# Optimization experiments

Measured on AMD Instinct MI355X. Metric: run time of the kernel, lower is better.

## Reference

```python
import jax, jax.numpy as jnp
import numpy as np

N = 50000          # num nodes
E = 400000         # num edges
D_NODE = 128       # num_inputs_node
D_EDGE = 32        # num_inputs_edge
D_OUT = 128        # num_outputs
R = 16             # num_relations
B = 8              # num_bases


def setup_inputs() -> dict:
    key = jax.random.key(0)
    ks = jax.random.split(key, 12)
    s = 0.05  # small init scale (glorot-like)
    return {
        "vfts": jax.random.normal(ks[0], (N, D_NODE), dtype=jnp.float32),
        "adjs": jax.random.randint(ks[1], (2, E), 0, N, dtype=jnp.int32),
        "rels": jax.random.randint(ks[2], (E,), 0, R, dtype=jnp.int32),
        "embed_rels": jax.random.normal(ks[3], (E, D_EDGE), dtype=jnp.float32),
        "embed_rels_target": jax.random.normal(ks[4], (E, D_EDGE), dtype=jnp.float32),
        "weight": jax.random.normal(ks[5], (B, D_NODE, D_OUT), dtype=jnp.float32) * s,
        "comp": jax.random.normal(ks[6], (R, B), dtype=jnp.float32) * s,
        "attn_w1": jax.random.normal(ks[7], (2 * D_NODE + 2 * D_EDGE, D_OUT), dtype=jnp.float32) * s,
        "attn_b1": jnp.zeros((D_OUT,), dtype=jnp.float32),
        "attn_w2": jax.random.normal(ks[8], (D_OUT, 1), dtype=jnp.float32) * s,
        "attn_b2": jnp.zeros((1,), dtype=jnp.float32),
        "update": jax.random.normal(ks[9], (D_NODE, D_OUT), dtype=jnp.float32) * s,
    }


def reference(vfts, adjs, rels, embed_rels, embed_rels_target,
              weight, comp, attn_w1, attn_b1, attn_w2, attn_b2, update):
    src, dst = adjs[0], adjs[1]
    # per-edge attention: concat(src feat, dst feat, rel embed, rel-target embed) -> [E, 2*Dn+2*De]
    erps = jnp.concatenate((vfts[src], vfts[dst], embed_rels, embed_rels_target), axis=1)
    h = jax.nn.relu(erps @ attn_w1 + attn_b1)
    alphas = jax.nn.sigmoid(h @ attn_w2 + attn_b2)  # [E, 1]
    # basis-decomposed relation weights: [R, D_NODE, D_OUT]
    w_rel = (comp @ weight.reshape(B, D_NODE * D_OUT)).reshape(R, D_NODE, D_OUT)
    # dense broadcast matmul as in original: [R, N, D_OUT]
    srcs_dense = jnp.einsum('nd,rdo->rno', vfts, w_rel)
    # gather (rel, src) pairs, scale by alphas gathered BY RELATION INDEX (faithful to original alphas[rels])
    srcs = alphas[rels] * srcs_dense[rels, src]  # [E, D_OUT]
    vrps = jnp.zeros((vfts.shape[0], D_OUT), dtype=vfts.dtype)
    vrps = vrps.at[dst].add(srcs)
    dsts = vfts @ update  # [N, D_OUT]
    vrps = vrps.at[dst].add(dsts[dst])  # self-update added once per incoming edge
    return jax.nn.relu(vrps)
```

## Files before the change

### kernel.cpp

```cpp
#include <hip/hip_runtime.h>
#include <hip/hip_bf16.h>

#define D 128
#define DE 32
#define RNUM 16
#define BNUM 8
#define APAD 132
#define EPB 32
#define NBLK 256
#define PPART 32

typedef __attribute__((ext_vector_type(8))) short bfrag8;
typedef __attribute__((ext_vector_type(4))) float facc4;

__device__ inline unsigned short f2bf(float f) {
    union { float f; unsigned int u; } v; v.f = f;
    unsigned int u = v.u + 0x7FFFu + ((v.u >> 16) & 1u);
    return (unsigned short)(u >> 16);
}
__device__ inline float bf2f(unsigned short h) {
    union { unsigned int u; float f; } v; v.u = ((unsigned int)h) << 16; return v.f;
}

__global__ void k_wrel(const float* __restrict__ comp, const float* __restrict__ weight,
                       float* __restrict__ wrel) {
    int idx = blockIdx.x * blockDim.x + threadIdx.x;
    int total = RNUM * D * D;
    int stride = gridDim.x * blockDim.x;
    for (; idx < total; idx += stride) {
        int r = idx >> 14;
        int rest = idx & 16383;
        float s = 0.f;
#pragma unroll
        for (int b = 0; b < BNUM; ++b) s += comp[r * BNUM + b] * weight[b * 16384 + rest];
        wrel[idx] = s;
    }
}

__global__ void k_alphas(const float* __restrict__ vfts, const int* __restrict__ adjs,
                         const float* __restrict__ er, const float* __restrict__ ert,
                         const float* __restrict__ w1, const float* __restrict__ b1,
                         const float* __restrict__ w2, const float* __restrict__ b2,
                         float* __restrict__ alphas, int E) {
    __shared__ float erps[2 * D + 2 * DE];
    __shared__ float red[D];
    int e = blockIdx.x, t = threadIdx.x;
    int src = adjs[e], dst = adjs[E + e];
    erps[t] = vfts[src * D + t];
    erps[D + t] = vfts[dst * D + t];
    if (t < DE) {
        erps[2 * D + t] = er[e * DE + t];
        erps[2 * D + DE + t] = ert[e * DE + t];
    }
    __syncthreads();
    float h = b1[t];
    for (int k = 0; k < 2 * D + 2 * DE; ++k) h += erps[k] * w1[k * D + t];
    h = fmaxf(h, 0.f);
    red[t] = h * w2[t];
    __syncthreads();
    for (int s = 64; s > 0; s >>= 1) {
        if (t < s) red[t] += red[t + s];
        __syncthreads();
    }
    if (t == 0) alphas[e] = 1.f / (1.f + expf(-(red[0] + b2[0])));
}

__global__ void k_prep(const float* __restrict__ vfts, unsigned short* __restrict__ vb,
                       int total8) {
    int i = blockIdx.x * blockDim.x + threadIdx.x;
    int stride = gridDim.x * blockDim.x;
    for (; i < total8; i += stride) {
        float4 f0 = ((const float4*)vfts)[i * 2];
        float4 f1 = ((const float4*)vfts)[i * 2 + 1];
        bfrag8 v;
        v[0] = (short)f2bf(f0.x); v[1] = (short)f2bf(f0.y);
        v[2] = (short)f2bf(f0.z); v[3] = (short)f2bf(f0.w);
        v[4] = (short)f2bf(f1.x); v[5] = (short)f2bf(f1.y);
        v[6] = (short)f2bf(f1.z); v[7] = (short)f2bf(f1.w);
        ((bfrag8*)vb)[i] = v;
    }
}

__global__ void k_hist(const int* __restrict__ adjs, const int* __restrict__ rels, int E,
                       int* __restrict__ blockHist, int* __restrict__ indeg) {
    __shared__ int h[4][RNUM];
    int t = threadIdx.x;
    if (t < 4 * RNUM) ((int*)h)[t] = 0;
    __syncthreads();
    int w = t >> 6;
    int chunk = (E + NBLK - 1) / NBLK;
    int start = blockIdx.x * chunk;
    int end = min(start + chunk, E);
    for (int i = start + t; i < end; i += 256) {
        atomicAdd(&h[w][rels[i]], 1);
        atomicAdd(&indeg[adjs[E + i]], 1);
    }
    __syncthreads();
    if (t < RNUM)
        blockHist[blockIdx.x * RNUM + t] = h[0][t] + h[1][t] + h[2][t] + h[3][t];
}

__global__ void k_prefix2(const int* __restrict__ blockHist, int* __restrict__ basep,
                          int* __restrict__ blockBase) {
    __shared__ int hist[NBLK * RNUM];
    __shared__ int pre[NBLK * RNUM];
    __shared__ int bp[RNUM + 1];
    int t = threadIdx.x;
    for (int i = t; i < NBLK * RNUM; i += 256) hist[i] = blockHist[i];
    __syncthreads();
    if (t < RNUM) {
        int s = 0;
        for (int b = 0; b < NBLK; ++b) {
            pre[b * RNUM + t] = s;
            s += hist[b * RNUM + t];
        }
        bp[t] = s;
    }
    __syncthreads();
    if (t == 0) {
        int s = 0;
        for (int r = 0; r < RNUM; ++r) {
            int c = bp[r];
            bp[r] = s;
            basep[r] = s;
            s += c;
        }
        bp[RNUM] = s;
        basep[RNUM] = s;
    }
    __syncthreads();
    for (int i = t; i < NBLK * RNUM; i += 256)
        blockBase[i] = pre[i] + bp[i & (RNUM - 1)];
}

__global__ void k_scatter2(const int* __restrict__ rels, int E,
                           const int* __restrict__ blockBase, int* __restrict__ sorted) {
    __shared__ int pos[RNUM];
    int t = threadIdx.x;
    if (t < RNUM) pos[t] = blockBase[blockIdx.x * RNUM + t];
    __syncthreads();
    int chunk = (E + NBLK - 1) / NBLK;
    int start = blockIdx.x * chunk;
    int end = min(start + chunk, E);
    for (int i = start + t; i < end; i += 256) {
        int p = atomicAdd(&pos[rels[i]], 1);
        sorted[p] = i;
    }
}

__global__ void k_scanA(const int* __restrict__ indeg, int N, int* __restrict__ chunkSum) {
    __shared__ int sc[256];
    int t = threadIdx.x;
    int chunk = (N + NBLK - 1) / NBLK;
    int n0 = blockIdx.x * chunk;
    int v = (t < chunk && n0 + t < N) ? indeg[n0 + t] : 0;
    sc[t] = v;
    __syncthreads();
    for (int s = 128; s > 0; s >>= 1) {
        if (t < s) sc[t] += sc[t + s];
        __syncthreads();
    }
    if (t == 0) chunkSum[blockIdx.x] = sc[0];
}

__global__ void k_scanB(const int* __restrict__ chunkSum, int* __restrict__ chunkBase,
                        int* __restrict__ dstbase, int N) {
    if (threadIdx.x == 0) {
        int s = 0;
        for (int b = 0; b < NBLK; ++b) {
            chunkBase[b] = s;
            s += chunkSum[b];
        }
        dstbase[N] = s;
    }
}

__global__ void k_scanC(const int* __restrict__ indeg, int N,
                        const int* __restrict__ chunkBase, int* __restrict__ dstbase,
                        int* __restrict__ dpos) {
    __shared__ int sc[256];
    int t = threadIdx.x;
    int chunk = (N + NBLK - 1) / NBLK;
    int n0 = blockIdx.x * chunk;
    bool valid = (t < chunk) && (n0 + t < N);
    int v = valid ? indeg[n0 + t] : 0;
    sc[t] = v;
    __syncthreads();
    for (int ofs = 1; ofs < 256; ofs <<= 1) {
        int x = (t >= ofs) ? sc[t - ofs] : 0;
        __syncthreads();
        sc[t] += x;
        __syncthreads();
    }
    if (valid) {
        int excl = chunkBase[blockIdx.x] + sc[t] - v;
        dstbase[n0 + t] = excl;
        dpos[n0 + t] = excl;
    }
}

__global__ void k_dstpos(const int* __restrict__ adjs, const int* __restrict__ sorted, int E,
                         int* __restrict__ dpos, int* __restrict__ possorted) {
    int i = blockIdx.x * blockDim.x + threadIdx.x;
    int stride = gridDim.x * blockDim.x;
    for (; i < E; i += stride) {
        int eid = sorted[i];
        int dst = adjs[E + eid];
        possorted[i] = atomicAdd(&dpos[dst], 1);
    }
}

__global__ void __launch_bounds__(512)
k_edge(const unsigned short* __restrict__ vb, const int* __restrict__ adjs,
       const float* __restrict__ wrel, const float* __restrict__ alphas,
       const int* __restrict__ basep, const int* __restrict__ sorted,
       const int* __restrict__ possorted, unsigned short* __restrict__ srcs16, int E) {
    __shared__ unsigned short wt[D * D];
    __shared__ unsigned short at[EPB * D];
    __shared__ int esrc[EPB], epos[EPB];
    int t = threadIdx.x;
    int r = blockIdx.x / PPART;
    int bp = blockIdx.x % PPART;

    const float* wr = wrel + r * D * D;
    for (int i = t; i < D * D; i += 512) {
        int k = i >> 7, col = i & 127;
        int byte = (col << 8) + (k << 1);
        byte ^= (col & 7) << 4;
        *(unsigned short*)((char*)wt + byte) = f2bf(wr[i]);
    }
    float alpha = alphas[r];
    int s0 = basep[r], s1 = basep[r + 1];

    int lane = t & 63;
    int wave = t >> 6;
    int mtile = wave >> 2;
    int colbase = (wave & 3) << 5;
    int se = t >> 4;
    int skb = (t & 15) << 3;

    for (int off = s0 + bp * EPB; off < s1; off += PPART * EPB) {
        __syncthreads();
        if (t < EPB) {
            int idx = off + t;
            if (idx < s1) {
                int eid = sorted[idx];
                esrc[t] = adjs[eid];
                epos[t] = possorted[idx];
            } else {
                esrc[t] = 0;
                epos[t] = -1;
            }
        }
        __syncthreads();
        {
            bfrag8 v = *(const bfrag8*)(vb + (size_t)esrc[se] * D + skb);
            int byte = (se << 8) + (skb << 1);
            byte ^= (se & 7) << 4;
            *(bfrag8*)((char*)at + byte) = v;
        }
        __syncthreads();

        facc4 acc0 = {0.f, 0.f, 0.f, 0.f}, acc1 = {0.f, 0.f, 0.f, 0.f};
        int eb = (mtile << 4) + (lane & 15);
        int c0 = colbase + (lane & 15);
        int c1 = c0 + 16;
#pragma unroll
        for (int kk = 0; kk < 4; ++kk) {
            int kbase = (kk << 5) + ((lane >> 4) << 3);
            int ab = ((eb << 8) + (kbase << 1)) ^ ((eb & 7) << 4);
            bfrag8 a = *(const bfrag8*)((char*)at + ab);
            int b0 = ((c0 << 8) + (kbase << 1)) ^ ((c0 & 7) << 4);
            bfrag8 bv0 = *(const bfrag8*)((char*)wt + b0);
            int b1 = ((c1 << 8) + (kbase << 1)) ^ ((c1 & 7) << 4);
            bfrag8 bv1 = *(const bfrag8*)((char*)wt + b1);
            acc0 = __builtin_amdgcn_mfma_f32_16x16x32_bf16(a, bv0, acc0, 0, 0, 0);
            acc1 = __builtin_amdgcn_mfma_f32_16x16x32_bf16(a, bv1, acc1, 0, 0, 0);
        }
        int ebase = (mtile << 4) + ((lane >> 4) << 2);
#pragma unroll
        for (int j = 0; j < 4; ++j) {
            int p = epos[ebase + j];
            if (p >= 0) {
                unsigned short* q = srcs16 + (size_t)p * D + c0;
                q[0]  = f2bf(alpha * acc0[j]);
                q[16] = f2bf(alpha * acc1[j]);
            }
        }
    }
}

#define INIT_NODES 16
__global__ void __launch_bounds__(256)
k_final(const float* __restrict__ vfts, const float* __restrict__ update,
        const int* __restrict__ dstbase, const unsigned short* __restrict__ srcs16,
        float* __restrict__ out, int N) {
    __shared__ float upd[D * D];
    __shared__ float rows[INIT_NODES][APAD];
    int t = threadIdx.x;
    for (int idx = t; idx < D * D; idx += 256) upd[idx] = update[idx];
    int g = t >> 5;
    int cg = t & 31;
    for (int nb = blockIdx.x * INIT_NODES; nb < N; nb += gridDim.x * INIT_NODES) {
        __syncthreads();
        for (int idx = t; idx < INIT_NODES * D; idx += 256) {
            int nn = idx >> 7, k = idx & 127;
            int n = nb + nn;
            rows[nn][k] = (n < N) ? vfts[n * D + k] : 0.f;
        }
        __syncthreads();
        int n0 = g * 2, n1 = g * 2 + 1;
        float acc0[4] = {0, 0, 0, 0}, acc1[4] = {0, 0, 0, 0};
#pragma unroll 4
        for (int k = 0; k < D; ++k) {
            float4 w = *(const float4*)&upd[k * D + cg * 4];
            float a0 = rows[n0][k], a1 = rows[n1][k];
            acc0[0] += a0 * w.x; acc0[1] += a0 * w.y; acc0[2] += a0 * w.z; acc0[3] += a0 * w.w;
            acc1[0] += a1 * w.x; acc1[1] += a1 * w.y; acc1[2] += a1 * w.z; acc1[3] += a1 * w.w;
        }
        int na = nb + n0, nc = nb + n1;
        if (na < N) {
            int b0 = dstbase[na], b1 = dstbase[na + 1];
            float deg = (float)(b1 - b0);
            float r0 = deg * acc0[0], r1 = deg * acc0[1], r2 = deg * acc0[2], r3 = deg * acc0[3];
            for (int p = b0; p < b1; ++p) {
                ushort4 u = *(const ushort4*)(srcs16 + (size_t)p * D + cg * 4);
                r0 += bf2f(u.x); r1 += bf2f(u.y); r2 += bf2f(u.z); r3 += bf2f(u.w);
            }
            *(float4*)&out[(size_t)na * D + cg * 4] =
                make_float4(fmaxf(r0, 0.f), fmaxf(r1, 0.f), fmaxf(r2, 0.f), fmaxf(r3, 0.f));
        }
        if (nc < N) {
            int b0 = dstbase[nc], b1 = dstbase[nc + 1];
            float deg = (float)(b1 - b0);
            float r0 = deg * acc1[0], r1 = deg * acc1[1], r2 = deg * acc1[2], r3 = deg * acc1[3];
            for (int p = b0; p < b1; ++p) {
                ushort4 u = *(const ushort4*)(srcs16 + (size_t)p * D + cg * 4);
                r0 += bf2f(u.x); r1 += bf2f(u.y); r2 += bf2f(u.z); r3 += bf2f(u.w);
            }
            *(float4*)&out[(size_t)nc * D + cg * 4] =
                make_float4(fmaxf(r0, 0.f), fmaxf(r1, 0.f), fmaxf(r2, 0.f), fmaxf(r3, 0.f));
        }
    }
}

__global__ void k_init(const float* __restrict__ vfts, const float* __restrict__ update,
                       const int* __restrict__ indeg, float* __restrict__ out, int N) {
    __shared__ float upd[D * D];
    __shared__ float rows[INIT_NODES][APAD];
    int t = threadIdx.x;
    for (int idx = t; idx < D * D; idx += 256) upd[idx] = update[idx];
    int g = t >> 5;
    int cg = t & 31;
    for (int nb = blockIdx.x * INIT_NODES; nb < N; nb += gridDim.x * INIT_NODES) {
        __syncthreads();
        for (int idx = t; idx < INIT_NODES * D; idx += 256) {
            int nn = idx >> 7, k = idx & 127;
            int n = nb + nn;
            rows[nn][k] = (n < N) ? vfts[n * D + k] : 0.f;
        }
        __syncthreads();
        int n0 = g * 2, n1 = g * 2 + 1;
        float acc0[4] = {0, 0, 0, 0}, acc1[4] = {0, 0, 0, 0};
#pragma unroll 4
        for (int k = 0; k < D; ++k) {
            float4 w = *(const float4*)&upd[k * D + cg * 4];
            float a0 = rows[n0][k], a1 = rows[n1][k];
            acc0[0] += a0 * w.x; acc0[1] += a0 * w.y; acc0[2] += a0 * w.z; acc0[3] += a0 * w.w;
            acc1[0] += a1 * w.x; acc1[1] += a1 * w.y; acc1[2] += a1 * w.z; acc1[3] += a1 * w.w;
        }
        int na = nb + n0, nc = nb + n1;
        if (na < N) {
            float deg = (float)indeg[na];
            *(float4*)&out[na * D + cg * 4] =
                make_float4(deg * acc0[0], deg * acc0[1], deg * acc0[2], deg * acc0[3]);
        }
        if (nc < N) {
            float deg = (float)indeg[nc];
            *(float4*)&out[nc * D + cg * 4] =
                make_float4(deg * acc1[0], deg * acc1[1], deg * acc1[2], deg * acc1[3]);
        }
    }
}

__global__ void __launch_bounds__(512)
k_edge_at(const float* __restrict__ vfts, const int* __restrict__ adjs,
          const float* __restrict__ wrel, const float* __restrict__ alphas,
          const int* __restrict__ basep, const int* __restrict__ sorted,
          float* __restrict__ out, int E) {
    __shared__ unsigned short wt[D * D];
    __shared__ unsigned short at[EPB * D];
    __shared__ int esrc[EPB], edst[EPB];
    int t = threadIdx.x;
    int r = blockIdx.x / PPART;
    int bp = blockIdx.x % PPART;
    const float* wr = wrel + r * D * D;
    for (int i = t; i < D * D; i += 512) {
        int k = i >> 7, col = i & 127;
        int byte = (col << 8) + (k << 1);
        byte ^= (col & 7) << 4;
        *(unsigned short*)((char*)wt + byte) = f2bf(wr[i]);
    }
    float alpha = alphas[r];
    int s0 = basep[r], s1 = basep[r + 1];
    int lane = t & 63;
    int wave = t >> 6;
    int mtile = wave >> 2;
    int colbase = (wave & 3) << 5;
    int se = t >> 4;
    int skb = (t & 15) << 3;
    for (int off = s0 + bp * EPB; off < s1; off += PPART * EPB) {
        __syncthreads();
        if (t < EPB) {
            int idx = off + t;
            if (idx < s1) {
                int eid = sorted[idx];
                esrc[t] = adjs[eid];
                edst[t] = adjs[E + eid];
            } else {
                esrc[t] = 0;
                edst[t] = -1;
            }
        }
        __syncthreads();
        {
            const float* sp = vfts + (size_t)esrc[se] * D + skb;
            float4 f0 = *(const float4*)sp;
            float4 f1 = *(const float4*)(sp + 4);
            bfrag8 v;
            v[0] = (short)f2bf(f0.x); v[1] = (short)f2bf(f0.y);
            v[2] = (short)f2bf(f0.z); v[3] = (short)f2bf(f0.w);
            v[4] = (short)f2bf(f1.x); v[5] = (short)f2bf(f1.y);
            v[6] = (short)f2bf(f1.z); v[7] = (short)f2bf(f1.w);
            int byte = (se << 8) + (skb << 1);
            byte ^= (se & 7) << 4;
            *(bfrag8*)((char*)at + byte) = v;
        }
        __syncthreads();
        facc4 acc0 = {0.f, 0.f, 0.f, 0.f}, acc1 = {0.f, 0.f, 0.f, 0.f};
        int eb = (mtile << 4) + (lane & 15);
        int c0 = colbase + (lane & 15);
        int c1 = c0 + 16;
#pragma unroll
        for (int kk = 0; kk < 4; ++kk) {
            int kbase = (kk << 5) + ((lane >> 4) << 3);
            int ab = ((eb << 8) + (kbase << 1)) ^ ((eb & 7) << 4);
            bfrag8 a = *(const bfrag8*)((char*)at + ab);
            int b0 = ((c0 << 8) + (kbase << 1)) ^ ((c0 & 7) << 4);
            bfrag8 bv0 = *(const bfrag8*)((char*)wt + b0);
            int b1 = ((c1 << 8) + (kbase << 1)) ^ ((c1 & 7) << 4);
            bfrag8 bv1 = *(const bfrag8*)((char*)wt + b1);
            acc0 = __builtin_amdgcn_mfma_f32_16x16x32_bf16(a, bv0, acc0, 0, 0, 0);
            acc1 = __builtin_amdgcn_mfma_f32_16x16x32_bf16(a, bv1, acc1, 0, 0, 0);
        }
        int ebase = (mtile << 4) + ((lane >> 4) << 2);
#pragma unroll
        for (int j = 0; j < 4; ++j) {
            int d = edst[ebase + j];
            if (d >= 0) {
                float* p = out + (size_t)d * D + c0;
                atomicAdd(p, alpha * acc0[j]);
                atomicAdd(p + 16, alpha * acc1[j]);
            }
        }
    }
}

__global__ void k_relu(float* __restrict__ out, int total4) {
    int i = blockIdx.x * blockDim.x + threadIdx.x;
    int stride = gridDim.x * blockDim.x;
    for (; i < total4; i += stride) {
        float4 v = ((float4*)out)[i];
        v.x = fmaxf(v.x, 0.f);
        v.y = fmaxf(v.y, 0.f);
        v.z = fmaxf(v.z, 0.f);
        v.w = fmaxf(v.w, 0.f);
        ((float4*)out)[i] = v;
    }
}

extern "C" void kernel_launch(void* const* d_in, const int* in_sizes, int n_in,
                              void* d_out, int out_size, void* d_ws, size_t ws_size,
                              hipStream_t stream) {
    const float* vfts   = (const float*)d_in[0];
    const int*   adjs   = (const int*)d_in[1];
    const int*   rels   = (const int*)d_in[2];
    const float* er     = (const float*)d_in[3];
    const float* ert    = (const float*)d_in[4];
    const float* weight = (const float*)d_in[5];
    const float* comp   = (const float*)d_in[6];
    const float* w1     = (const float*)d_in[7];
    const float* b1     = (const float*)d_in[8];
    const float* w2     = (const float*)d_in[9];
    const float* b2     = (const float*)d_in[10];
    const float* update = (const float*)d_in[11];
    float* out = (float*)d_out;

    int N = in_sizes[0] / D;
    int E = in_sizes[2];
    int Nr = (N + 63) & ~63;

    char* ws = (char*)d_ws;
    size_t o = 0;
    float* wrel = (float*)(ws + o);            o += (size_t)RNUM * D * D * 4;
    float* alphas = (float*)(ws + o);          o += 256;
    unsigned short* vb = (unsigned short*)(ws + o);     o += (size_t)N * D * 2;
    o = (o + 255) & ~(size_t)255;
    unsigned short* srcs16 = (unsigned short*)(ws + o); o += (size_t)E * D * 2;
    o = (o + 255) & ~(size_t)255;
    int* basep     = (int*)(ws + o);           o += 128;
    int* indeg     = (int*)(ws + o);           o += (size_t)Nr * 4;
    int* blockHist = (int*)(ws + o);           o += (size_t)NBLK * RNUM * 4;
    int* blockBase = (int*)(ws + o);           o += (size_t)NBLK * RNUM * 4;
    int* sorted    = (int*)(ws + o);           o += (size_t)E * 4;
    int* chunkSum  = (int*)(ws + o);           o += NBLK * 4;
    int* chunkBase = (int*)(ws + o);           o += NBLK * 4;
    int* dstbase   = (int*)(ws + o);           o += (size_t)(Nr + 64) * 4;
    int* dpos      = (int*)(ws + o);           o += (size_t)Nr * 4;
    int* possorted = (int*)(ws + o);           o += (size_t)E * 4;
    bool big = (o <= ws_size);

    if (big) {
        hipMemsetAsync(indeg, 0, (size_t)Nr * 4, stream);
        k_wrel<<<256, 256, 0, stream>>>(comp, weight, wrel);
        k_alphas<<<RNUM, D, 0, stream>>>(vfts, adjs, er, ert, w1, b1, w2, b2, alphas, E);
        k_prep<<<1024, 256, 0, stream>>>(vfts, vb, N * D / 8);
        k_hist<<<NBLK, 256, 0, stream>>>(adjs, rels, E, blockHist, indeg);
        k_prefix2<<<1, 256, 0, stream>>>(blockHist, basep, blockBase);
        k_scatter2<<<NBLK, 256, 0, stream>>>(rels, E, blockBase, sorted);
        k_scanA<<<NBLK, 256, 0, stream>>>(indeg, N, chunkSum);
        k_scanB<<<1, 64, 0, stream>>>(chunkSum, chunkBase, dstbase, N);
        k_scanC<<<NBLK, 256, 0, stream>>>(indeg, N, chunkBase, dstbase, dpos);
        k_dstpos<<<256, 256, 0, stream>>>(adjs, sorted, E, dpos, possorted);
        k_edge<<<RNUM * PPART, 512, 0, stream>>>(vb, adjs, wrel, alphas, basep, sorted,
                                                 possorted, srcs16, E);
        k_final<<<512, 256, 0, stream>>>(vfts, update, dstbase, srcs16, out, N);
    } else {
        float* fwrel   = (float*)ws;
        float* falphas = (float*)(ws + (1 << 20));
        int* ib = (int*)(ws + (1 << 20) + 256);
        int* fbasep     = ib;
        int* findeg     = ib + 32;
        int* fblockHist = findeg + Nr;
        int* fblockBase = fblockHist + NBLK * RNUM;
        int* fsorted    = fblockBase + NBLK * RNUM;

        hipMemsetAsync(findeg, 0, (size_t)Nr * 4, stream);
        k_wrel<<<256, 256, 0, stream>>>(comp, weight, fwrel);
        k_alphas<<<RNUM, D, 0, stream>>>(vfts, adjs, er, ert, w1, b1, w2, b2, falphas, E);
        k_hist<<<NBLK, 256, 0, stream>>>(adjs, rels, E, fblockHist, findeg);
        k_prefix2<<<1, 256, 0, stream>>>(fblockHist, fbasep, fblockBase);
        k_scatter2<<<NBLK, 256, 0, stream>>>(rels, E, fblockBase, fsorted);
        k_init<<<512, 256, 0, stream>>>(vfts, update, findeg, out, N);
        k_edge_at<<<RNUM * PPART, 512, 0, stream>>>(vfts, adjs, fwrel, falphas, fbasep,
                                                    fsorted, out, E);
        k_relu<<<512, 256, 0, stream>>>(out, N * D / 4);
    }
}
```

Measured before the change: 379.7 us.

## Split final kernel into MFMA self-update GEMM and wave-per-node segment sum

The fused fp32 final kernel is replaced by two kernels. The first computes vfts@update with bf16 MFMA into the output buffer before the edge kernel runs. The second assigns one wave per destination node to sum its bf16 edge rows with coalesced 4-byte loads, adding degree times the stored self-update and applying ReLU. This moves the self-update off scalar fp32 FMAs and improves coalescing of the segment sum. In exchange it adds an extra write and read of the output, plus bf16 rounding of the self-update term.

Measured after the change: 321.4 us. 1.18x faster.

```diff
diff --git a/kernel.cpp b/kernel.cpp
--- a/kernel.cpp
+++ b/kernel.cpp
@@ -290,60 +290,93 @@
     }
 }
 
+__global__ void __launch_bounds__(512)
+k_dsts(const unsigned short* __restrict__ vb, const float* __restrict__ update,
+       float* __restrict__ out, int N) {
+    __shared__ unsigned short wt[D * D];
+    __shared__ unsigned short at[32 * D];
+    int t = threadIdx.x;
+    for (int i = t; i < D * D; i += 512) {
+        int k = i >> 7, col = i & 127;
+        int byte = (col << 8) + (k << 1);
+        byte ^= (col & 7) << 4;
+        *(unsigned short*)((char*)wt + byte) = f2bf(update[i]);
+    }
+    int lane = t & 63;
+    int wave = t >> 6;
+    int mtile = wave >> 2;
+    int colbase = (wave & 3) << 5;
+    int se = t >> 4;
+    int skb = (t & 15) << 3;
+    int nb = blockIdx.x * 32;
+    {
+        int n = nb + se;
+        if (n >= N) n = N - 1;
+        bfrag8 v = *(const bfrag8*)(vb + (size_t)n * D + skb);
+        int byte = ((se << 8) + (skb << 1)) ^ ((se & 7) << 4);
+        *(bfrag8*)((char*)at + byte) = v;
+    }
+    __syncthreads();
+    facc4 acc0 = {0.f, 0.f, 0.f, 0.f}, acc1 = {0.f, 0.f, 0.f, 0.f};
+    int eb = (mtile << 4) + (lane & 15);
+    int c0 = colbase + (lane & 15);
+    int c1 = c0 + 16;
+#pragma unroll
+    for (int kk = 0; kk < 4; ++kk) {
+        int kbase = (kk << 5) + ((lane >> 4) << 3);
+        int ab = ((eb << 8) + (kbase << 1)) ^ ((eb & 7) << 4);
+        bfrag8 a = *(const bfrag8*)((char*)at + ab);
+        int b0 = ((c0 << 8) + (kbase << 1)) ^ ((c0 & 7) << 4);
+        bfrag8 bv0 = *(const bfrag8*)((char*)wt + b0);
+        int b1 = ((c1 << 8) + (kbase << 1)) ^ ((c1 & 7) << 4);
+        bfrag8 bv1 = *(const bfrag8*)((char*)wt + b1);
+        acc0 = __builtin_amdgcn_mfma_f32_16x16x32_bf16(a, bv0, acc0, 0, 0, 0);
+        acc1 = __builtin_amdgcn_mfma_f32_16x16x32_bf16(a, bv1, acc1, 0, 0, 0);
+    }
+    int ebase = (mtile << 4) + ((lane >> 4) << 2);
+#pragma unroll
+    for (int j = 0; j < 4; ++j) {
+        int n = nb + ebase + j;
+        if (n < N) {
+            float* q = out + (size_t)n * D + c0;
+            q[0]  = acc0[j];
+            q[16] = acc1[j];
+        }
+    }
+}
+
+__global__ void __launch_bounds__(256)
+k_sum(const int* __restrict__ dstbase, const unsigned short* __restrict__ srcs16,
+      float* __restrict__ out, int N) {
+    int wid = (blockIdx.x * 256 + threadIdx.x) >> 6;
+    int lane = threadIdx.x & 63;
+    if (wid >= N) return;
+    int b0 = dstbase[wid], b1 = dstbase[wid + 1];
+    float deg = (float)(b1 - b0);
+    const unsigned int* base = (const unsigned int*)srcs16;
+    float a0 = 0.f, a1 = 0.f;
+    int p = b0;
+    for (; p + 4 <= b1; p += 4) {
+        unsigned int u0 = base[(size_t)(p + 0) * 64 + lane];
+        unsigned int u1 = base[(size_t)(p + 1) * 64 + lane];
+        unsigned int u2 = base[(size_t)(p + 2) * 64 + lane];
+        unsigned int u3 = base[(size_t)(p + 3) * 64 + lane];
+        a0 += bf2f((unsigned short)u0) + bf2f((unsigned short)u1) +
+              bf2f((unsigned short)u2) + bf2f((unsigned short)u3);
+        a1 += bf2f((unsigned short)(u0 >> 16)) + bf2f((unsigned short)(u1 >> 16)) +
+              bf2f((unsigned short)(u2 >> 16)) + bf2f((unsigned short)(u3 >> 16));
+    }
+    for (; p < b1; ++p) {
+        unsigned int u = base[(size_t)p * 64 + lane];
+        a0 += bf2f((unsigned short)u);
+        a1 += bf2f((unsigned short)(u >> 16));
+    }
+    float2* op = (float2*)out + (size_t)wid * 64 + lane;
+    float2 d = *op;
+    *op = make_float2(fmaxf(deg * d.x + a0, 0.f), fmaxf(deg * d.y + a1, 0.f));
+}
+
 #define INIT_NODES 16
-__global__ void __launch_bounds__(256)
-k_final(const float* __restrict__ vfts, const float* __restrict__ update,
-        const int* __restrict__ dstbase, const unsigned short* __restrict__ srcs16,
-        float* __restrict__ out, int N) {
-    __shared__ float upd[D * D];
-    __shared__ float rows[INIT_NODES][APAD];
-    int t = threadIdx.x;
-    for (int idx = t; idx < D * D; idx += 256) upd[idx] = update[idx];
-    int g = t >> 5;
-    int cg = t & 31;
-    for (int nb = blockIdx.x * INIT_NODES; nb < N; nb += gridDim.x * INIT_NODES) {
-        __syncthreads();
-        for (int idx = t; idx < INIT_NODES * D; idx += 256) {
-            int nn = idx >> 7, k = idx & 127;
-            int n = nb + nn;
-            rows[nn][k] = (n < N) ? vfts[n * D + k] : 0.f;
-        }
-        __syncthreads();
-        int n0 = g * 2, n1 = g * 2 + 1;
-        float acc0[4] = {0, 0, 0, 0}, acc1[4] = {0, 0, 0, 0};
-#pragma unroll 4
-        for (int k = 0; k < D; ++k) {
-            float4 w = *(const float4*)&upd[k * D + cg * 4];
-            float a0 = rows[n0][k], a1 = rows[n1][k];
-            acc0[0] += a0 * w.x; acc0[1] += a0 * w.y; acc0[2] += a0 * w.z; acc0[3] += a0 * w.w;
-            acc1[0] += a1 * w.x; acc1[1] += a1 * w.y; acc1[2] += a1 * w.z; acc1[3] += a1 * w.w;
-        }
-        int na = nb + n0, nc = nb + n1;
-        if (na < N) {
-            int b0 = dstbase[na], b1 = dstbase[na + 1];
-            float deg = (float)(b1 - b0);
-            float r0 = deg * acc0[0], r1 = deg * acc0[1], r2 = deg * acc0[2], r3 = deg * acc0[3];
-            for (int p = b0; p < b1; ++p) {
-                ushort4 u = *(const ushort4*)(srcs16 + (size_t)p * D + cg * 4);
-                r0 += bf2f(u.x); r1 += bf2f(u.y); r2 += bf2f(u.z); r3 += bf2f(u.w);
-            }
-            *(float4*)&out[(size_t)na * D + cg * 4] =
-                make_float4(fmaxf(r0, 0.f), fmaxf(r1, 0.f), fmaxf(r2, 0.f), fmaxf(r3, 0.f));
-        }
-        if (nc < N) {
-            int b0 = dstbase[nc], b1 = dstbase[nc + 1];
-            float deg = (float)(b1 - b0);
-            float r0 = deg * acc1[0], r1 = deg * acc1[1], r2 = deg * acc1[2], r3 = deg * acc1[3];
-            for (int p = b0; p < b1; ++p) {
-                ushort4 u = *(const ushort4*)(srcs16 + (size_t)p * D + cg * 4);
-                r0 += bf2f(u.x); r1 += bf2f(u.y); r2 += bf2f(u.z); r3 += bf2f(u.w);
-            }
-            *(float4*)&out[(size_t)nc * D + cg * 4] =
-                make_float4(fmaxf(r0, 0.f), fmaxf(r1, 0.f), fmaxf(r2, 0.f), fmaxf(r3, 0.f));
-        }
-    }
-}
-
 __global__ void k_init(const float* __restrict__ vfts, const float* __restrict__ update,
                        const int* __restrict__ indeg, float* __restrict__ out, int N) {
     __shared__ float upd[D * D];
@@ -532,9 +565,10 @@
         k_scanB<<<1, 64, 0, stream>>>(chunkSum, chunkBase, dstbase, N);
         k_scanC<<<NBLK, 256, 0, stream>>>(indeg, N, chunkBase, dstbase, dpos);
         k_dstpos<<<256, 256, 0, stream>>>(adjs, sorted, E, dpos, possorted);
+        k_dsts<<<(N + 31) / 32, 512, 0, stream>>>(vb, update, out, N);
         k_edge<<<RNUM * PPART, 512, 0, stream>>>(vb, adjs, wrel, alphas, basep, sorted,
                                                  possorted, srcs16, E);
-        k_final<<<512, 256, 0, stream>>>(vfts, update, dstbase, srcs16, out, N);
+        k_sum<<<(N + 3) / 4, 256, 0, stream>>>(dstbase, srcs16, out, N);
     } else {
         float* fwrel   = (float*)ws;
         float* falphas = (float*)(ws + (1 << 20));
```

## Aggregate basis-projected features per node then apply one concatenated basis GEMM

Applied to the files above, without the earlier changes.

Replaces the per-edge, per-relation matmul (sort by relation, compute E×128 projected rows, then sum per destination) with an algebraic reordering. Each destination node first sums its source features into 8 basis-coefficient-weighted accumulators, and one MFMA GEMM against the concatenated 8 basis weights plus the update matrix then produces the output. This removes the relation sort, the E×D bf16 intermediate buffer and the E-row matmul, cutting the matmul to N rows with K=9×128. The costs are a bf16 aggregation buffer of N×1024 and a rounding of the per-node sums to bf16 before the GEMM, which may change numerical accuracy.

Result: faster. 304.7 us (-19.8%).

```diff
diff --git a/kernel.cpp b/kernel.cpp
--- a/kernel.cpp
+++ b/kernel.cpp
@@ -20,21 +20,6 @@
 }
 __device__ inline float bf2f(unsigned short h) {
     union { unsigned int u; float f; } v; v.u = ((unsigned int)h) << 16; return v.f;
-}
-
-__global__ void k_wrel(const float* __restrict__ comp, const float* __restrict__ weight,
-                       float* __restrict__ wrel) {
-    int idx = blockIdx.x * blockDim.x + threadIdx.x;
-    int total = RNUM * D * D;
-    int stride = gridDim.x * blockDim.x;
-    for (; idx < total; idx += stride) {
-        int r = idx >> 14;
-        int rest = idx & 16383;
-        float s = 0.f;
-#pragma unroll
-        for (int b = 0; b < BNUM; ++b) s += comp[r * BNUM + b] * weight[b * 16384 + rest];
-        wrel[idx] = s;
-    }
 }
 
 __global__ void k_alphas(const float* __restrict__ vfts, const int* __restrict__ adjs,
@@ -65,6 +50,26 @@
     if (t == 0) alphas[e] = 1.f / (1.f + expf(-(red[0] + b2[0])));
 }
 
+__global__ void k_coef(const float* __restrict__ alphas, const float* __restrict__ comp,
+                       float* __restrict__ coef) {
+    int t = threadIdx.x;
+    if (t < RNUM * BNUM) coef[t] = alphas[t >> 3] * comp[t];
+}
+
+__global__ void k_wcat(const float* __restrict__ weight, const float* __restrict__ update,
+                       unsigned short* __restrict__ wcatT) {
+    int idx = blockIdx.x * blockDim.x + threadIdx.x;
+    int total = 9 * D * D;
+    int stride = gridDim.x * blockDim.x;
+    for (; idx < total; idx += stride) {
+        int s = idx >> 14;
+        int rest = idx & 16383;
+        int col = rest >> 7, k = rest & 127;
+        float v = (s < 8) ? weight[s * 16384 + k * D + col] : update[k * D + col];
+        wcatT[idx] = f2bf(v);
+    }
+}
+
 __global__ void k_prep(const float* __restrict__ vfts, unsigned short* __restrict__ vb,
                        int total8) {
     int i = blockIdx.x * blockDim.x + threadIdx.x;
@@ -81,6 +86,221 @@
     }
 }
 
+__global__ void k_indeg(const int* __restrict__ adjs, int E, int* __restrict__ indeg) {
+    int i = blockIdx.x * blockDim.x + threadIdx.x;
+    int stride = gridDim.x * blockDim.x;
+    for (; i < E; i += stride) atomicAdd(&indeg[adjs[E + i]], 1);
+}
+
+__global__ void k_scanA(const int* __restrict__ indeg, int N, int* __restrict__ chunkSum) {
+    __shared__ int sc[256];
+    int t = threadIdx.x;
+    int chunk = (N + NBLK - 1) / NBLK;
+    int n0 = blockIdx.x * chunk;
+    int v = (t < chunk && n0 + t < N) ? indeg[n0 + t] : 0;
+    sc[t] = v;
+    __syncthreads();
+    for (int s = 128; s > 0; s >>= 1) {
+        if (t < s) sc[t] += sc[t + s];
+        __syncthreads();
+    }
+    if (t == 0) chunkSum[blockIdx.x] = sc[0];
+}
+
+__global__ void k_scanB(const int* __restrict__ chunkSum, int* __restrict__ chunkBase,
+                        int* __restrict__ dstbase, int N) {
+    if (threadIdx.x == 0) {
+        int s = 0;
+        for (int b = 0; b < NBLK; ++b) {
+            chunkBase[b] = s;
+            s += chunkSum[b];
+        }
+        dstbase[N] = s;
+    }
+}
+
+__global__ void k_scanC(const int* __restrict__ indeg, int N,
+                        const int* __restrict__ chunkBase, int* __restrict__ dstbase,
+                        int* __restrict__ dpos) {
+    __shared__ int sc[256];
+    int t = threadIdx.x;
+    int chunk = (N + NBLK - 1) / NBLK;
+    int n0 = blockIdx.x * chunk;
+    bool valid = (t < chunk) && (n0 + t < N);
+    int v = valid ? indeg[n0 + t] : 0;
+    sc[t] = v;
+    __syncthreads();
+    for (int ofs = 1; ofs < 256; ofs <<= 1) {
+        int x = (t >= ofs) ? sc[t - ofs] : 0;
+        __syncthreads();
+        sc[t] += x;
+        __syncthreads();
+    }
+    if (valid) {
+        int excl = chunkBase[blockIdx.x] + sc[t] - v;
+        dstbase[n0 + t] = excl;
+        dpos[n0 + t] = excl;
+    }
+}
+
+__global__ void k_dstscatter(const int* __restrict__ adjs, const int* __restrict__ rels, int E,
+                             int* __restrict__ dpos, int2* __restrict__ srcrel) {
+    int i = blockIdx.x * blockDim.x + threadIdx.x;
+    int stride = gridDim.x * blockDim.x;
+    for (; i < E; i += stride) {
+        int dst = adjs[E + i];
+        int p = atomicAdd(&dpos[dst], 1);
+        srcrel[p] = make_int2(adjs[i], rels[i]);
+    }
+}
+
+__global__ void __launch_bounds__(256)
+k_agg(const unsigned short* __restrict__ vb, const int2* __restrict__ srcrel,
+      const int* __restrict__ dstbase, const float* __restrict__ coef,
+      unsigned short* __restrict__ aggc, int N) {
+    __shared__ float cs[RNUM * BNUM];
+    int t = threadIdx.x;
+    if (t < RNUM * BNUM) cs[t] = coef[t];
+    __syncthreads();
+    int wid = (blockIdx.x * 256 + t) >> 6;
+    int lane = t & 63;
+    if (wid >= N) return;
+    int b0 = dstbase[wid], b1 = dstbase[wid + 1];
+    const unsigned int* vbd = (const unsigned int*)vb;
+    float a0_0 = 0, a0_1 = 0, a1_0 = 0, a1_1 = 0, a2_0 = 0, a2_1 = 0, a3_0 = 0, a3_1 = 0;
+    float a4_0 = 0, a4_1 = 0, a5_0 = 0, a5_1 = 0, a6_0 = 0, a6_1 = 0, a7_0 = 0, a7_1 = 0;
+    int p = b0;
+    for (; p + 2 <= b1; p += 2) {
+        int2 sr0 = srcrel[p];
+        int2 sr1 = srcrel[p + 1];
+        unsigned int u0 = vbd[(size_t)sr0.x * 64 + lane];
+        unsigned int u1 = vbd[(size_t)sr1.x * 64 + lane];
+        float4 cA0 = *(const float4*)&cs[sr0.y * 8];
+        float4 cB0 = *(const float4*)&cs[sr0.y * 8 + 4];
+        float4 cA1 = *(const float4*)&cs[sr1.y * 8];
+        float4 cB1 = *(const float4*)&cs[sr1.y * 8 + 4];
+        float v0 = bf2f((unsigned short)u0), v1 = bf2f((unsigned short)(u0 >> 16));
+        float w0 = bf2f((unsigned short)u1), w1 = bf2f((unsigned short)(u1 >> 16));
+        a0_0 += cA0.x * v0 + cA1.x * w0; a0_1 += cA0.x * v1 + cA1.x * w1;
+        a1_0 += cA0.y * v0 + cA1.y * w0; a1_1 += cA0.y * v1 + cA1.y * w1;
+        a2_0 += cA0.z * v0 + cA1.z * w0; a2_1 += cA0.z * v1 + cA1.z * w1;
+        a3_0 += cA0.w * v0 + cA1.w * w0; a3_1 += cA0.w * v1 + cA1.w * w1;
+        a4_0 += cB0.x * v0 + cB1.x * w0; a4_1 += cB0.x * v1 + cB1.x * w1;
+        a5_0 += cB0.y * v0 + cB1.y * w0; a5_1 += cB0.y * v1 + cB1.y * w1;
+        a6_0 += cB0.z * v0 + cB1.z * w0; a6_1 += cB0.z * v1 + cB1.z * w1;
+        a7_0 += cB0.w * v0 + cB1.w * w0; a7_1 += cB0.w * v1 + cB1.w * w1;
+    }
+    if (p < b1) {
+        int2 sr0 = srcrel[p];
+        unsigned int u0 = vbd[(size_t)sr0.x * 64 + lane];
+        float4 cA0 = *(const float4*)&cs[sr0.y * 8];
+        float4 cB0 = *(const float4*)&cs[sr0.y * 8 + 4];
+        float v0 = bf2f((unsigned short)u0), v1 = bf2f((unsigned short)(u0 >> 16));
+        a0_0 += cA0.x * v0; a0_1 += cA0.x * v1;
+        a1_0 += cA0.y * v0; a1_1 += cA0.y * v1;
+        a2_0 += cA0.z * v0; a2_1 += cA0.z * v1;
+        a3_0 += cA0.w * v0; a3_1 += cA0.w * v1;
+        a4_0 += cB0.x * v0; a4_1 += cB0.x * v1;
+        a5_0 += cB0.y * v0; a5_1 += cB0.y * v1;
+        a6_0 += cB0.z * v0; a6_1 += cB0.z * v1;
+        a7_0 += cB0.w * v0; a7_1 += cB0.w * v1;
+    }
+    unsigned int* ob = (unsigned int*)(aggc + (size_t)wid * 1024);
+#define PACK(x, y) ((unsigned int)f2bf(x) | ((unsigned int)f2bf(y) << 16))
+    ob[0 * 64 + lane] = PACK(a0_0, a0_1);
+    ob[1 * 64 + lane] = PACK(a1_0, a1_1);
+    ob[2 * 64 + lane] = PACK(a2_0, a2_1);
+    ob[3 * 64 + lane] = PACK(a3_0, a3_1);
+    ob[4 * 64 + lane] = PACK(a4_0, a4_1);
+    ob[5 * 64 + lane] = PACK(a5_0, a5_1);
+    ob[6 * 64 + lane] = PACK(a6_0, a6_1);
+    ob[7 * 64 + lane] = PACK(a7_0, a7_1);
+#undef PACK
+}
+
+__global__ void __launch_bounds__(512)
+k_gemm(const unsigned short* __restrict__ aggc, const unsigned short* __restrict__ vb,
+       const unsigned short* __restrict__ wcatT, const int* __restrict__ dstbase,
+       float* __restrict__ out, int N) {
+    __shared__ unsigned short wt[D * D];
+    __shared__ unsigned short at[32 * D];
+    int t = threadIdx.x;
+    int lane = t & 63;
+    int wave = t >> 6;
+    int mtile = wave >> 2;
+    int colbase = (wave & 3) << 5;
+    int se = t >> 4;
+    int skb = (t & 15) << 3;
+    int nb = blockIdx.x * 32;
+    int nclamp = min(nb + se, N - 1);
+    facc4 accA0 = {0, 0, 0, 0}, accA1 = {0, 0, 0, 0};
+    facc4 accB0 = {0, 0, 0, 0}, accB1 = {0, 0, 0, 0};
+    int eb = (mtile << 4) + (lane & 15);
+    int c0 = colbase + (lane & 15);
+    int c1 = c0 + 16;
+    int wcol = t >> 4;
+    int wkb = (t & 15) << 3;
+    for (int s = 0; s < 9; ++s) {
+        __syncthreads();
+#pragma unroll
+        for (int q = 0; q < 4; ++q) {
+            int col = wcol + (q << 5);
+            bfrag8 v = *(const bfrag8*)(wcatT + (size_t)s * 16384 + col * D + wkb);
+            int byte = ((col << 8) + (wkb << 1)) ^ ((col & 7) << 4);
+            *(bfrag8*)((char*)wt + byte) = v;
+        }
+        {
+            const unsigned short* src = (s < 8)
+                ? aggc + (size_t)nclamp * 1024 + s * D + skb
+                : vb + (size_t)nclamp * D + skb;
+            bfrag8 v = *(const bfrag8*)src;
+            int byte = ((se << 8) + (skb << 1)) ^ ((se & 7) << 4);
+            *(bfrag8*)((char*)at + byte) = v;
+        }
+        __syncthreads();
+#pragma unroll
+        for (int kk = 0; kk < 4; ++kk) {
+            int kbase = (kk << 5) + ((lane >> 4) << 3);
+            bfrag8 a = *(const bfrag8*)((char*)at + (((eb << 8) + (kbase << 1)) ^ ((eb & 7) << 4)));
+            bfrag8 bv0 = *(const bfrag8*)((char*)wt + (((c0 << 8) + (kbase << 1)) ^ ((c0 & 7) << 4)));
+            bfrag8 bv1 = *(const bfrag8*)((char*)wt + (((c1 << 8) + (kbase << 1)) ^ ((c1 & 7) << 4)));
+            if (s < 8) {
+                accA0 = __builtin_amdgcn_mfma_f32_16x16x32_bf16(a, bv0, accA0, 0, 0, 0);
+                accA1 = __builtin_amdgcn_mfma_f32_16x16x32_bf16(a, bv1, accA1, 0, 0, 0);
+            } else {
+                accB0 = __builtin_amdgcn_mfma_f32_16x16x32_bf16(a, bv0, accB0, 0, 0, 0);
+                accB1 = __builtin_amdgcn_mfma_f32_16x16x32_bf16(a, bv1, accB1, 0, 0, 0);
+            }
+        }
+    }
+    int ebase = (mtile << 4) + ((lane >> 4) << 2);
+#pragma unroll
+    for (int j = 0; j < 4; ++j) {
+        int n = nb + ebase + j;
+        if (n < N) {
+            float deg = (float)(dstbase[n + 1] - dstbase[n]);
+            float* q = out + (size_t)n * D + c0;
+            q[0]  = fmaxf(accA0[j] + deg * accB0[j], 0.f);
+            q[16] = fmaxf(accA1[j] + deg * accB1[j], 0.f);
+        }
+    }
+}
+
+__global__ void k_wrel(const float* __restrict__ comp, const float* __restrict__ weight,
+                       float* __restrict__ wrel) {
+    int idx = blockIdx.x * blockDim.x + threadIdx.x;
+    int total = RNUM * D * D;
+    int stride = gridDim.x * blockDim.x;
+    for (; idx < total; idx += stride) {
+        int r = idx >> 14;
+        int rest = idx & 16383;
+        float s = 0.f;
+#pragma unroll
+        for (int b = 0; b < BNUM; ++b) s += comp[r * BNUM + b] * weight[b * 16384 + rest];
+        wrel[idx] = s;
+    }
+}
+
 __global__ void k_hist(const int* __restrict__ adjs, const int* __restrict__ rels, int E,
                        int* __restrict__ blockHist, int* __restrict__ indeg) {
     __shared__ int h[4][RNUM];
@@ -148,202 +368,7 @@
     }
 }
 
-__global__ void k_scanA(const int* __restrict__ indeg, int N, int* __restrict__ chunkSum) {
-    __shared__ int sc[256];
-    int t = threadIdx.x;
-    int chunk = (N + NBLK - 1) / NBLK;
-    int n0 = blockIdx.x * chunk;
-    int v = (t < chunk && n0 + t < N) ? indeg[n0 + t] : 0;
-    sc[t] = v;
-    __syncthreads();
-    for (int s = 128; s > 0; s >>= 1) {
-        if (t < s) sc[t] += sc[t + s];
-        __syncthreads();
-    }
-    if (t == 0) chunkSum[blockIdx.x] = sc[0];
-}
-
-__global__ void k_scanB(const int* __restrict__ chunkSum, int* __restrict__ chunkBase,
-                        int* __restrict__ dstbase, int N) {
-    if (threadIdx.x == 0) {
-        int s = 0;
-        for (int b = 0; b < NBLK; ++b) {
-            chunkBase[b] = s;
-            s += chunkSum[b];
-        }
-        dstbase[N] = s;
-    }
-}
-
-__global__ void k_scanC(const int* __restrict__ indeg, int N,
-                        const int* __restrict__ chunkBase, int* __restrict__ dstbase,
-                        int* __restrict__ dpos) {
-    __shared__ int sc[256];
-    int t = threadIdx.x;
-    int chunk = (N + NBLK - 1) / NBLK;
-    int n0 = blockIdx.x * chunk;
-    bool valid = (t < chunk) && (n0 + t < N);
-    int v = valid ? indeg[n0 + t] : 0;
-    sc[t] = v;
-    __syncthreads();
-    for (int ofs = 1; ofs < 256; ofs <<= 1) {
-        int x = (t >= ofs) ? sc[t - ofs] : 0;
-        __syncthreads();
-        sc[t] += x;
-        __syncthreads();
-    }
-    if (valid) {
-        int excl = chunkBase[blockIdx.x] + sc[t] - v;
-        dstbase[n0 + t] = excl;
-        dpos[n0 + t] = excl;
-    }
-}
-
-__global__ void k_dstpos(const int* __restrict__ adjs, const int* __restrict__ sorted, int E,
-                         int* __restrict__ dpos, int* __restrict__ possorted) {
-    int i = blockIdx.x * blockDim.x + threadIdx.x;
-    int stride = gridDim.x * blockDim.x;
-    for (; i < E; i += stride) {
-        int eid = sorted[i];
-        int dst = adjs[E + eid];
-        possorted[i] = atomicAdd(&dpos[dst], 1);
-    }
-}
-
-__global__ void __launch_bounds__(512)
-k_edge(const unsigned short* __restrict__ vb, const int* __restrict__ adjs,
-       const float* __restrict__ wrel, const float* __restrict__ alphas,
-       const int* __restrict__ basep, const int* __restrict__ sorted,
-       const int* __restrict__ possorted, unsigned short* __restrict__ srcs16, int E) {
-    __shared__ unsigned short wt[D * D];
-    __shared__ unsigned short at[EPB * D];
-    __shared__ int esrc[EPB], epos[EPB];
-    int t = threadIdx.x;
-    int r = blockIdx.x / PPART;
-    int bp = blockIdx.x % PPART;
-
-    const float* wr = wrel + r * D * D;
-    for (int i = t; i < D * D; i += 512) {
-        int k = i >> 7, col = i & 127;
-        int byte = (col << 8) + (k << 1);
-        byte ^= (col & 7) << 4;
-        *(unsigned short*)((char*)wt + byte) = f2bf(wr[i]);
-    }
-    float alpha = alphas[r];
-    int s0 = basep[r], s1 = basep[r + 1];
-
-    int lane = t & 63;
-    int wave = t >> 6;
-    int mtile = wave >> 2;
-    int colbase = (wave & 3) << 5;
-    int se = t >> 4;
-    int skb = (t & 15) << 3;
-
-    for (int off = s0 + bp * EPB; off < s1; off += PPART * EPB) {
-        __syncthreads();
-        if (t < EPB) {
-            int idx = off + t;
-            if (idx < s1) {
-                int eid = sorted[idx];
-                esrc[t] = adjs[eid];
-                epos[t] = possorted[idx];
-            } else {
-                esrc[t] = 0;
-                epos[t] = -1;
-            }
-        }
-        __syncthreads();
-        {
-            bfrag8 v = *(const bfrag8*)(vb + (size_t)esrc[se] * D + skb);
-            int byte = (se << 8) + (skb << 1);
-            byte ^= (se & 7) << 4;
-            *(bfrag8*)((char*)at + byte) = v;
-        }
-        __syncthreads();
-
-        facc4 acc0 = {0.f, 0.f, 0.f, 0.f}, acc1 = {0.f, 0.f, 0.f, 0.f};
-        int eb = (mtile << 4) + (lane & 15);
-        int c0 = colbase + (lane & 15);
-        int c1 = c0 + 16;
-#pragma unroll
-        for (int kk = 0; kk < 4; ++kk) {
-            int kbase = (kk << 5) + ((lane >> 4) << 3);
-            int ab = ((eb << 8) + (kbase << 1)) ^ ((eb & 7) << 4);
-            bfrag8 a = *(const bfrag8*)((char*)at + ab);
-            int b0 = ((c0 << 8) + (kbase << 1)) ^ ((c0 & 7) << 4);
-            bfrag8 bv0 = *(const bfrag8*)((char*)wt + b0);
-            int b1 = ((c1 << 8) + (kbase << 1)) ^ ((c1 & 7) << 4);
-            bfrag8 bv1 = *(const bfrag8*)((char*)wt + b1);
-            acc0 = __builtin_amdgcn_mfma_f32_16x16x32_bf16(a, bv0, acc0, 0, 0, 0);
-            acc1 = __builtin_amdgcn_mfma_f32_16x16x32_bf16(a, bv1, acc1, 0, 0, 0);
-        }
-        int ebase = (mtile << 4) + ((lane >> 4) << 2);
-#pragma unroll
-        for (int j = 0; j < 4; ++j) {
-            int p = epos[ebase + j];
-            if (p >= 0) {
-                unsigned short* q = srcs16 + (size_t)p * D + c0;
-                q[0]  = f2bf(alpha * acc0[j]);
-                q[16] = f2bf(alpha * acc1[j]);
-            }
-        }
-    }
-}
-
 #define INIT_NODES 16
-__global__ void __launch_bounds__(256)
-k_final(const float* __restrict__ vfts, const float* __restrict__ update,
-        const int* __restrict__ dstbase, const unsigned short* __restrict__ srcs16,
-        float* __restrict__ out, int N) {
-    __shared__ float upd[D * D];
-    __shared__ float rows[INIT_NODES][APAD];
-    int t = threadIdx.x;
-    for (int idx = t; idx < D * D; idx += 256) upd[idx] = update[idx];
-    int g = t >> 5;
-    int cg = t & 31;
-    for (int nb = blockIdx.x * INIT_NODES; nb < N; nb += gridDim.x * INIT_NODES) {
-        __syncthreads();
-        for (int idx = t; idx < INIT_NODES * D; idx += 256) {
-            int nn = idx >> 7, k = idx & 127;
-            int n = nb + nn;
-            rows[nn][k] = (n < N) ? vfts[n * D + k] : 0.f;
-        }
-        __syncthreads();
-        int n0 = g * 2, n1 = g * 2 + 1;
-        float acc0[4] = {0, 0, 0, 0}, acc1[4] = {0, 0, 0, 0};
-#pragma unroll 4
-        for (int k = 0; k < D; ++k) {
-            float4 w = *(const float4*)&upd[k * D + cg * 4];
-            float a0 = rows[n0][k], a1 = rows[n1][k];
-            acc0[0] += a0 * w.x; acc0[1] += a0 * w.y; acc0[2] += a0 * w.z; acc0[3] += a0 * w.w;
-            acc1[0] += a1 * w.x; acc1[1] += a1 * w.y; acc1[2] += a1 * w.z; acc1[3] += a1 * w.w;
-        }
-        int na = nb + n0, nc = nb + n1;
-        if (na < N) {
-            int b0 = dstbase[na], b1 = dstbase[na + 1];
-            float deg = (float)(b1 - b0);
-            float r0 = deg * acc0[0], r1 = deg * acc0[1], r2 = deg * acc0[2], r3 = deg * acc0[3];
-            for (int p = b0; p < b1; ++p) {
-                ushort4 u = *(const ushort4*)(srcs16 + (size_t)p * D + cg * 4);
-                r0 += bf2f(u.x); r1 += bf2f(u.y); r2 += bf2f(u.z); r3 += bf2f(u.w);
-            }
-            *(float4*)&out[(size_t)na * D + cg * 4] =
-                make_float4(fmaxf(r0, 0.f), fmaxf(r1, 0.f), fmaxf(r2, 0.f), fmaxf(r3, 0.f));
-        }
-        if (nc < N) {
-            int b0 = dstbase[nc], b1 = dstbase[nc + 1];
-            float deg = (float)(b1 - b0);
-            float r0 = deg * acc1[0], r1 = deg * acc1[1], r2 = deg * acc1[2], r3 = deg * acc1[3];
-            for (int p = b0; p < b1; ++p) {
-                ushort4 u = *(const ushort4*)(srcs16 + (size_t)p * D + cg * 4);
-                r0 += bf2f(u.x); r1 += bf2f(u.y); r2 += bf2f(u.z); r3 += bf2f(u.w);
-            }
-            *(float4*)&out[(size_t)nc * D + cg * 4] =
-                make_float4(fmaxf(r0, 0.f), fmaxf(r1, 0.f), fmaxf(r2, 0.f), fmaxf(r3, 0.f));
-        }
-    }
-}
-
 __global__ void k_init(const float* __restrict__ vfts, const float* __restrict__ update,
                        const int* __restrict__ indeg, float* __restrict__ out, int N) {
     __shared__ float upd[D * D];
@@ -502,39 +527,35 @@
 
     char* ws = (char*)d_ws;
     size_t o = 0;
-    float* wrel = (float*)(ws + o);            o += (size_t)RNUM * D * D * 4;
-    float* alphas = (float*)(ws + o);          o += 256;
-    unsigned short* vb = (unsigned short*)(ws + o);     o += (size_t)N * D * 2;
+    float* alphas = (float*)(ws + o);                    o += 256;
+    float* coef   = (float*)(ws + o);                    o += 512 + 256;
+    unsigned short* vb = (unsigned short*)(ws + o);      o += (size_t)N * D * 2;
     o = (o + 255) & ~(size_t)255;
-    unsigned short* srcs16 = (unsigned short*)(ws + o); o += (size_t)E * D * 2;
+    unsigned short* aggc = (unsigned short*)(ws + o);    o += (size_t)N * 1024 * 2;
     o = (o + 255) & ~(size_t)255;
-    int* basep     = (int*)(ws + o);           o += 128;
-    int* indeg     = (int*)(ws + o);           o += (size_t)Nr * 4;
-    int* blockHist = (int*)(ws + o);           o += (size_t)NBLK * RNUM * 4;
-    int* blockBase = (int*)(ws + o);           o += (size_t)NBLK * RNUM * 4;
-    int* sorted    = (int*)(ws + o);           o += (size_t)E * 4;
-    int* chunkSum  = (int*)(ws + o);           o += NBLK * 4;
-    int* chunkBase = (int*)(ws + o);           o += NBLK * 4;
-    int* dstbase   = (int*)(ws + o);           o += (size_t)(Nr + 64) * 4;
-    int* dpos      = (int*)(ws + o);           o += (size_t)Nr * 4;
-    int* possorted = (int*)(ws + o);           o += (size_t)E * 4;
+    unsigned short* wcatT = (unsigned short*)(ws + o);   o += (size_t)9 * D * D * 2;
+    o = (o + 255) & ~(size_t)255;
+    int2* srcrel   = (int2*)(ws + o);                    o += (size_t)E * 8;
+    int* indeg     = (int*)(ws + o);                     o += (size_t)Nr * 4;
+    int* dstbase   = (int*)(ws + o);                     o += (size_t)(Nr + 64) * 4;
+    int* dpos      = (int*)(ws + o);                     o += (size_t)Nr * 4;
+    int* chunkSum  = (int*)(ws + o);                     o += NBLK * 4;
+    int* chunkBase = (int*)(ws + o);                     o += NBLK * 4;
     bool big = (o <= ws_size);
 
     if (big) {
         hipMemsetAsync(indeg, 0, (size_t)Nr * 4, stream);
-        k_wrel<<<256, 256, 0, stream>>>(comp, weight, wrel);
         k_alphas<<<RNUM, D, 0, stream>>>(vfts, adjs, er, ert, w1, b1, w2, b2, alphas, E);
+        k_coef<<<1, 128, 0, stream>>>(alphas, comp, coef);
         k_prep<<<1024, 256, 0, stream>>>(vfts, vb, N * D / 8);
-        k_hist<<<NBLK, 256, 0, stream>>>(adjs, rels, E, blockHist, indeg);
-        k_prefix2<<<1, 256, 0, stream>>>(blockHist, basep, blockBase);
-        k_scatter2<<<NBLK, 256, 0, stream>>>(rels, E, blockBase, sorted);
+        k_wcat<<<256, 256, 0, stream>>>(weight, update, wcatT);
+        k_indeg<<<256, 256, 0, stream>>>(adjs, E, indeg);
         k_scanA<<<NBLK, 256, 0, stream>>>(indeg, N, chunkSum);
         k_scanB<<<1, 64, 0, stream>>>(chunkSum, chunkBase, dstbase, N);
         k_scanC<<<NBLK, 256, 0, stream>>>(indeg, N, chunkBase, dstbase, dpos);
-        k_dstpos<<<256, 256, 0, stream>>>(adjs, sorted, E, dpos, possorted);
-        k_edge<<<RNUM * PPART, 512, 0, stream>>>(vb, adjs, wrel, alphas, basep, sorted,
-                                                 possorted, srcs16, E);
-        k_final<<<512, 256, 0, stream>>>(vfts, update, dstbase, srcs16, out, N);
+        k_dstscatter<<<256, 256, 0, stream>>>(adjs, rels, E, dpos, srcrel);
+        k_agg<<<(N * 64 + 255) / 256, 256, 0, stream>>>(vb, srcrel, dstbase, coef, aggc, N);
+        k_gemm<<<(N + 31) / 32, 512, 0, stream>>>(aggc, vb, wcatT, dstbase, out, N);
     } else {
         float* fwrel   = (float*)ws;
         float* falphas = (float*)(ws + (1 << 20));
```
